# Kernel tuning notes

Hardware: AMD Instinct MI355X
Metric: run time of the kernel (lower is better)

## Reference

```python
import jax, jax.numpy as jnp
import numpy as np

NUM_CLASSES = 80
IGNORE_THRESH = 0.7
LOG_FLOOR = 1e-30  # guards log(0); only hit at masked positions where the BCE term is exactly zero


def _iou_cxcywh(a, b):
    # a: (N,4), b: (M,4), boxes as (cx,cy,w,h) -> IoU (N,M)
    tl = jnp.maximum(a[:, None, :2] - a[:, None, 2:] * 0.5,
                     b[None, :, :2] - b[None, :, 2:] * 0.5)
    br = jnp.minimum(a[:, None, :2] + a[:, None, 2:] * 0.5,
                     b[None, :, :2] + b[None, :, 2:] * 0.5)
    area_a = a[:, 2] * a[:, 3]
    area_b = b[:, 2] * b[:, 3]
    en = jnp.all(tl < br, axis=2).astype(a.dtype)
    area_i = jnp.prod(br - tl, axis=2) * en
    return area_i / (area_a[:, None] + area_b[None, :] - area_i)


def _safelog(x):
    return jnp.log(jnp.maximum(x, LOG_FLOOR))


def _bce_sum(p, t, w=None):
    l = -(t * _safelog(p) + (1.0 - t) * _safelog(1.0 - p))
    if w is not None:
        l = l * w
    return jnp.sum(l)


def _make_pred_boxes(outputs, masked_anchors, ref_anchors):
    B, C, H, W = outputs.shape
    A = masked_anchors.shape[0]
    nc = C // A - 5
    o = outputs.reshape(B, A, 5 + nc, H, W).transpose(0, 1, 3, 4, 2)  # (B,A,H,W,5+nc)
    xs = jnp.arange(W, dtype=o.dtype)
    ys = jnp.arange(H, dtype=o.dtype)
    bx = jax.nn.sigmoid(o[..., 0]) + xs[None, None, None, :]
    by = jax.nn.sigmoid(o[..., 1]) + ys[None, None, :, None]
    bw = jnp.exp(o[..., 2]) * masked_anchors[:, 0][None, :, None, None]
    bh = jnp.exp(o[..., 3]) * masked_anchors[:, 1][None, :, None, None]
    pred = jnp.stack([bx, by, bw, bh], axis=-1)             # (B,A,H,W,4)
    pred = pred.transpose(0, 2, 3, 1, 4).reshape(B, H * W, A, 4)
    gx, gy = jnp.meshgrid(xs, ys)                            # (H,W)
    grid = jnp.stack([gx, gy], axis=-1).reshape(H * W, 1, 2)
    masked_x1y1 = jnp.concatenate(
        [jnp.broadcast_to(grid, (H * W, A, 2)),
         jnp.broadcast_to(masked_anchors[None], (H * W, A, 2))], axis=-1)
    R = ref_anchors.shape[0]
    ref_grid = jnp.concatenate(
        [jnp.broadcast_to(grid, (H * W, R, 2)),
         jnp.broadcast_to(ref_anchors[None], (H * W, R, 2))], axis=-1)
    return pred, masked_x1y1, ref_grid


def _build_targets_one(pred_boxes, gt, num_obj, masked_x1y1, ref_xcyc, anchor_mask, H, W):
    HW = H * W
    A = masked_x1y1.shape[1]
    M = gt.shape[0]
    dtype = pred_boxes.dtype
    gt_boxes = gt[:, :4] * jnp.array([W, H, W, H], dtype=dtype)
    gt_cls = jnp.clip(gt[:, 4].astype(jnp.int32), 0, NUM_CLASSES - 1)
    valid = jnp.arange(M) < num_obj

    ious = _iou_cxcywh(pred_boxes.reshape(-1, 4), gt_boxes)  # (HW*A, M)
    ious = jnp.where(valid[None, :], ious, -1.0)
    max_iou = jnp.max(ious.reshape(HW, A, M), axis=-1)       # (HW, A)

    n_pos = jnp.sum(max_iou > IGNORE_THRESH)
    iou_mask0 = jnp.ones((HW, A), dtype)
    iou_mask0 = jnp.where((n_pos > 0) & (max_iou >= IGNORE_THRESH),
                          jnp.zeros((), dtype), iou_mask0)

    R = ref_xcyc.shape[1]
    ref_ious = _iou_cxcywh(ref_xcyc.reshape(-1, 4), gt_boxes).reshape(HW, R, M)

    init = dict(
        iou_target=jnp.zeros((HW, A), dtype),
        iou_mask=iou_mask0,
        box_target=jnp.zeros((HW, A, 4), dtype),
        box_mask=jnp.zeros((HW, A), dtype),
        box_scale=jnp.zeros((HW, A, 2), dtype),
        class_target=jnp.zeros((HW, A, NUM_CLASSES), dtype),
        class_mask=jnp.zeros((HW, A), dtype),
    )

    one = jnp.ones((), dtype)

    def body(state, xs):
        gt_box, cls_i, v, ref_iou_obj = xs       # ref_iou_obj: (HW, R)
        cx = jnp.floor(gt_box[0]).astype(jnp.int32)
        cy = jnp.floor(gt_box[1]).astype(jnp.int32)
        cell = jnp.clip(cy * W + cx, 0, HW - 1)
        aidx = jnp.argmax(ref_iou_obj[cell])
        do = v & jnp.any(aidx == anchor_mask)
        a3 = aidx % 3
        resp = masked_x1y1[cell, a3]
        delta = jnp.stack([gt_box[0] - resp[0], gt_box[1] - resp[1],
                           gt_box[2] / resp[2], gt_box[3] / resp[3]])
        scale = jnp.sqrt(2.0 - gt_box[2] * gt_box[3] / W / H)

        def upd(arr, new):
            old = arr[cell, a3]
            return arr.at[cell, a3].set(jnp.where(do, new, old))

        new_state = dict(
            iou_target=upd(state['iou_target'], max_iou[cell, a3]),
            iou_mask=upd(state['iou_mask'], one),
            box_target=upd(state['box_target'], delta),
            box_mask=upd(state['box_mask'], one),
            box_scale=upd(state['box_scale'], jnp.stack([scale, scale])),
            class_target=state['class_target'].at[cell, a3, cls_i].set(
                jnp.where(do, one, state['class_target'][cell, a3, cls_i])),
            class_mask=upd(state['class_mask'], one),
        )
        return new_state, None

    xs = (gt_boxes, gt_cls, valid, jnp.moveaxis(ref_ious, -1, 0))
    state, _ = jax.lax.scan(body, init, xs)
    state['iou_mask'] = jnp.where(num_obj == 0, jnp.zeros((), dtype), state['iou_mask'])
    return state


def _forward_loss(outputs, targets, masked_anchors, ref_anchors, anchor_mask):
    B, C, H, W = outputs.shape
    A = masked_anchors.shape[0]
    nc = NUM_CLASSES
    det = jax.lax.stop_gradient(outputs)  # torch: build_targets(outputs.detach().clone(), ...)
    pred_boxes, masked_x1y1, ref_grid = _make_pred_boxes(det, masked_anchors, ref_anchors)
    # faithful to torch's (H*W,3,12) view: +0.5 hits x,y of ref anchors 0,3,6 only
    ref_xcyc = ref_grid.at[:, 0::3, :2].add(0.5)
    gt_num = jnp.sum(jnp.sum(targets, axis=2) > 0, axis=1)
    am = jnp.asarray(anchor_mask, dtype=jnp.int32)
    build = lambda pb, gt, n: _build_targets_one(pb, gt, n, masked_x1y1, ref_xcyc, am, H, W)
    bt = jax.vmap(build)(pred_boxes, targets, gt_num)

    o = outputs.reshape(B, A, 5 + nc, H, W).transpose(0, 3, 4, 1, 2).reshape(B, -1, 5 + nc)
    txy = jax.nn.sigmoid(o[..., :2])
    twh = jnp.exp(o[..., 2:4])
    conf = jax.nn.sigmoid(o[..., 4])
    probs = jax.nn.sigmoid(o[..., 5:])

    box_mask = bt['box_mask'].reshape(-1, 1)
    box_target = bt['box_target'].reshape(-1, 4) * box_mask
    box_scale = bt['box_scale'].reshape(-1, 2) * box_mask
    pred_deltas = jnp.concatenate([txy, twh], -1).reshape(-1, 4) * box_mask

    box_xy_loss = _bce_sum(pred_deltas[:, :2], box_target[:, :2], w=box_scale * box_scale)
    box_wh_loss = jnp.sum((pred_deltas[:, 2:] * box_scale - box_target[:, 2:] * box_scale) ** 2) / 2.0

    iou_mask = bt['iou_mask'].reshape(-1)
    pred_confs = conf.reshape(-1) * iou_mask
    iou_target = bt['iou_target'].reshape(-1) * iou_mask
    iou_loss = _bce_sum(pred_confs, iou_target)

    class_mask = (bt['class_mask'].reshape(-1, 1) > 0).astype(outputs.dtype)
    pred_probs = probs.reshape(-1, nc) * class_mask
    class_target = bt['class_target'].reshape(-1, nc) * class_mask
    class_loss = _bce_sum(pred_probs, class_target)

    return box_xy_loss + box_wh_loss + iou_loss + class_loss


def setup_inputs() -> dict:
    key = jax.random.key(0)
    k1, k2, k3, k4, k5 = jax.random.split(key, 5)
    B, A, H, W, M = 16, 3, 85, 85, 50
    C = A * (5 + NUM_CLASSES)
    outputs = jax.random.normal(k1, (B, C, H, W), jnp.float32)
    cxcy = jax.random.uniform(k2, (B, M, 2), jnp.float32, 0.05, 0.95)
    wh = jax.random.uniform(k3, (B, M, 2), jnp.float32, 0.05, 0.4)
    cls = jax.random.randint(k4, (B, M, 1), 0, NUM_CLASSES).astype(jnp.float32)
    targets = jnp.concatenate([cxcy, wh, cls], axis=-1)
    nobj = jax.random.randint(k5, (B,), 0, M + 1)
    valid = (jnp.arange(M)[None, :] < nobj[:, None]).astype(jnp.float32)
    targets = targets * valid[..., None]
    anchors = jnp.array([[10, 13], [16, 30], [33, 23], [30, 61], [62, 45],
                         [59, 119], [116, 90], [156, 198], [373, 326]], jnp.float32)
    stride = 8.0
    ref_anchors = anchors / stride
    masked_anchors = ref_anchors[:3]
    anchor_mask = jnp.array([0, 1, 2], jnp.int32)
    return {'outputs': outputs, 'targets': targets, 'masked_anchors': masked_anchors,
            'ref_anchors': ref_anchors, 'anchor_mask': anchor_mask}


def reference(outputs, targets, masked_anchors, ref_anchors, anchor_mask):
    return _forward_loss(outputs, targets, masked_anchors, ref_anchors, anchor_mask)
```

## Files before the change

### kernel.cpp

```cpp
#include <hip/hip_runtime.h>
#include <math.h>

#define NUM_CLASSES 80
#define BB 16
#define AA 3
#define HH 85
#define WW 85
#define HW (HH*WW)
#define MM 50
#define CH (AA*(5+NUM_CLASSES))
#define BX ((HW + 255)/256)
#define NBA (BB*AA)
#define NBLK (BX*NBA)

__device__ __forceinline__ float sigmoidf_(float x){ return 1.0f/(1.0f+expf(-x)); }
__device__ __forceinline__ float softplus_(float x){
    return fmaxf(x, 0.0f) + log1pf(expf(-fabsf(x)));
}
__device__ __forceinline__ double atomicExchD(double* p, double v){
    unsigned long long old = atomicExch((unsigned long long*)p, __double_as_longlong(v));
    return __longlong_as_double(old);
}

__global__ void __launch_bounds__(256) k_all(
        const float* __restrict__ outputs,
        const float* __restrict__ targets,
        const float* __restrict__ masked_anchors,
        const float* __restrict__ ref_anchors,
        const int* __restrict__ anchor_mask,
        char* __restrict__ wsb,
        float* __restrict__ out)
{
    double* acc_l  = (double*)(wsb);
    double* acc_lc = (double*)(wsb + 2048);
    int*    posfl  = (int*)(wsb + 4096);
    unsigned int* colcnt = (unsigned int*)(wsb + 6144);
    unsigned int* cnt    = (unsigned int*)(wsb + 12288);

    __shared__ float s_gx1[MM], s_gy1[MM], s_gx2[MM], s_gy2[MM], s_garea[MM];
    __shared__ float s_delta[MM][4];
    __shared__ float s_scale[MM];
    __shared__ int   s_no;
    __shared__ int   s_win[256];
    __shared__ unsigned int s_cm[256][3];
    __shared__ double s_rl[4], s_rlc[4];
    __shared__ int   s_anyw[4];
    __shared__ int   s_prev;
    __shared__ double s_fa[16], s_fc[16];
    __shared__ int   s_fp[16];

    const int tid  = threadIdx.x;
    const int ba   = blockIdx.y;
    const int b    = ba / AA, a = ba % AA;
    const int base = blockIdx.x << 8;
    const int bid  = ba * BX + blockIdx.x;

    if (tid == 0){
        unsigned int v = __hip_atomic_load(&colcnt[ba*32], __ATOMIC_RELAXED,
                                           __HIP_MEMORY_SCOPE_AGENT);
        if (v >= (unsigned int)BX) atomicCAS(&colcnt[ba*32], v, 0u);
    }

    s_win[tid] = -1;
    s_cm[tid][0] = 0u; s_cm[tid][1] = 0u; s_cm[tid][2] = 0u;

    float g0=0.f,g1=0.f,g2=0.f,g3=0.f,g4=0.f;
    bool gflag = false;
    if (tid < MM){
        const float* g = targets + ((size_t)b*MM + tid)*5;
        g0=g[0]; g1=g[1]; g2=g[2]; g3=g[3]; g4=g[4];
        gflag = (g0+g1+g2+g3+g4) > 0.0f;
    }
    unsigned long long bal = __ballot(gflag);
    if (tid == 0) s_no = __popcll(bal);
    __syncthreads();
    const int no = s_no;

    if (tid < MM){
        float gx = g0*(float)WW, gy = g1*(float)HH, gw = g2*(float)WW, gh = g3*(float)HH;
        int cls = min(max((int)g4, 0), NUM_CLASSES-1);
        bool valid = (tid < no);
        int cx = (int)floorf(gx), cy = (int)floorf(gy);
        int cell = min(max(cy*WW + cx, 0), HW-1);
        float xg = (float)(cell % WW), yg = (float)(cell / WW);
        float gx1 = gx - gw*0.5f, gy1 = gy - gh*0.5f;
        float gx2 = gx + gw*0.5f, gy2 = gy + gh*0.5f;
        float garea = gw*gh;
        float bai = -1.0f, bun = 1.0f; int aidx = 0;
        for (int r = 0; r < 9; ++r){
            float off = (r % 3 == 0) ? 0.5f : 0.0f;
            float acx = xg + off, acy = yg + off;
            float aw = ref_anchors[2*r], ah = ref_anchors[2*r+1];
            float tlx = fmaxf(acx - aw*0.5f, gx1), tly = fmaxf(acy - ah*0.5f, gy1);
            float brx = fminf(acx + aw*0.5f, gx2), bry = fminf(acy + ah*0.5f, gy2);
            float ai = (tlx < brx && tly < bry) ? (brx - tlx)*(bry - tly) : 0.0f;
            float un = aw*ah + garea - ai;
            if (ai*bun > bai*un){ bai = ai; bun = un; aidx = r; }
        }
        bool dof = valid && (aidx == anchor_mask[0] || aidx == anchor_mask[1] || aidx == anchor_mask[2]);
        int a3 = aidx % 3;
        float mw = masked_anchors[2*a3], mh = masked_anchors[2*a3+1];
        s_gx1[tid] = gx1; s_gy1[tid] = gy1; s_gx2[tid] = gx2; s_gy2[tid] = gy2;
        s_garea[tid] = garea;
        s_delta[tid][0] = gx - xg; s_delta[tid][1] = gy - yg;
        s_delta[tid][2] = gw/mw;   s_delta[tid][3] = gh/mh;
        s_scale[tid] = sqrtf(2.0f - gw*gh/(float)WW/(float)HH);
        if (dof && a3 == a){
            int ci = cell - base;
            if (ci >= 0 && ci < 256){
                atomicMax(&s_win[ci], tid);
                atomicOr(&s_cm[ci][cls >> 5], 1u << (cls & 31));
            }
        }
    }
    __syncthreads();

    double l = 0.0, lc = 0.0;
    bool pos = false;
    const int hw = base + tid;
    if (hw < HW && no > 0){
        int xg = hw % WW, yg = hw / WW;
        size_t obase = ((size_t)(b*CH + a*(5+NUM_CLASSES)))*HW + hw;
        float o0 = outputs[obase];
        float o1 = outputs[obase + HW];
        float o2 = outputs[obase + 2*HW];
        float o3 = outputs[obase + 3*HW];
        float o4 = outputs[obase + 4*HW];
        float px = sigmoidf_(o0) + (float)xg;
        float py = sigmoidf_(o1) + (float)yg;
        float e2 = expf(o2), e3 = expf(o3);
        float pw = e2*masked_anchors[2*a], ph = e3*masked_anchors[2*a+1];
        float px1 = px - pw*0.5f, py1 = py - ph*0.5f;
        float px2 = px + pw*0.5f, py2 = py + ph*0.5f;
        float parea = pw*ph;
        float bax = 0.0f, bun = 1.0f;
        for (int m = 0; m < no; ++m){
            float tlx = fmaxf(px1, s_gx1[m]), tly = fmaxf(py1, s_gy1[m]);
            float brx = fminf(px2, s_gx2[m]), bry = fminf(py2, s_gy2[m]);
            float ai = (tlx < brx && tly < bry) ? (brx - tlx)*(bry - tly) : 0.0f;
            float un = parea + s_garea[m] - ai;
            if (ai*bun > bax*un){ bax = ai; bun = un; }
        }
        pos = (bax > 0.7f*bun);
        int win = s_win[tid];
        float sp4 = softplus_(o4);
        if (win >= 0){
            float mi = bax/bun;
            l += (double)(sp4 - mi*o4);
            float dx = s_delta[win][0], dy = s_delta[win][1];
            float dw = s_delta[win][2], dh = s_delta[win][3];
            float s = s_scale[win];
            float w2 = s*s;
            l += (double)((softplus_(o0) - dx*o0)*w2);
            l += (double)((softplus_(o1) - dy*o1)*w2);
            float d2 = e2*s - dw*s, d3 = e3*s - dh*s;
            l += 0.5*((double)(d2*d2) + (double)(d3*d3));
            unsigned int c0 = s_cm[tid][0], c1 = s_cm[tid][1], c2 = s_cm[tid][2];
            #pragma unroll 8
            for (int c = 0; c < NUM_CLASSES; ++c){
                float oc = outputs[obase + (size_t)(5+c)*HW];
                unsigned int w = (c < 32) ? c0 : ((c < 64) ? c1 : c2);
                float tt = ((w >> (c & 31)) & 1u) ? 1.0f : 0.0f;
                l += (double)(softplus_(oc) - tt*oc);
            }
        } else {
            if (bax >= 0.7f*bun) lc += (double)sp4;
            else                 l  += (double)sp4;
        }
    }

    for (int off = 32; off > 0; off >>= 1){
        l  += __shfl_down(l,  off);
        lc += __shfl_down(lc, off);
    }
    unsigned long long pbal = __ballot(pos);
    int wid = tid >> 6;
    if ((tid & 63) == 0){
        s_rl[wid] = l; s_rlc[wid] = lc; s_anyw[wid] = (pbal != 0ull) ? 1 : 0;
    }
    __syncthreads();
    if (tid == 0){
        double bl  = s_rl[0] + s_rl[1] + s_rl[2] + s_rl[3];
        double blc = s_rlc[0] + s_rlc[1] + s_rlc[2] + s_rlc[3];
        int anyp = s_anyw[0] | s_anyw[1] | s_anyw[2] | s_anyw[3];
        atomicAdd(&acc_l[(bid & 15)*16], bl);
        if (blc != 0.0) atomicAdd(&acc_lc[b*16], blc);
        if (anyp) atomicOr(&posfl[b*32], 1);
        __builtin_amdgcn_s_waitcnt(0);
        int prev = -1;
        unsigned int cp = atomicAdd(&colcnt[ba*32], 1u);
        if (cp == (unsigned int)(BX - 1)){
            unsigned int v = __hip_atomic_load(cnt, __ATOMIC_RELAXED,
                                              __HIP_MEMORY_SCOPE_AGENT);
            if (v >= (unsigned int)NBA) atomicCAS(cnt, v, 0u);
            prev = (int)atomicAdd(cnt, 1u);
        }
        s_prev = prev;
    }
    __syncthreads();

    if (s_prev == NBA - 1){
        if (tid < 16)      s_fa[tid]      = atomicExchD(&acc_l[tid*16], 0.0);
        else if (tid < 32) s_fc[tid - 16] = atomicExchD(&acc_lc[(tid-16)*16], 0.0);
        else if (tid < 48) s_fp[tid - 32] = atomicExch(&posfl[(tid-32)*32], 0);
        else if (tid < 96) atomicExch(&colcnt[(tid-48)*32], 0u);
        __syncthreads();
        if (tid == 0){
            double t = 0.0;
            for (int i = 0; i < 16; ++i) t += s_fa[i];
            for (int bb = 0; bb < BB; ++bb) if (!s_fp[bb]) t += s_fc[bb];
            out[0] = (float)t;
            atomicExch(cnt, 0u);
        }
    }
}

extern "C" void kernel_launch(void* const* d_in, const int* in_sizes, int n_in,
                              void* d_out, int out_size, void* d_ws, size_t ws_size,
                              hipStream_t stream) {
    const float* outputs        = (const float*)d_in[0];
    const float* targets        = (const float*)d_in[1];
    const float* masked_anchors = (const float*)d_in[2];
    const float* ref_anchors    = (const float*)d_in[3];
    const int*   anchor_mask    = (const int*)d_in[4];

    dim3 grid(BX, NBA);
    k_all<<<grid, 256, 0, stream>>>(outputs, targets, masked_anchors, ref_anchors,
                                    anchor_mask, (char*)d_ws, (float*)d_out);
}
```

Baseline: 21.09 us.

## Use division-free IoU threshold test, float4 shared boxes, and 512-thread blocks

Replaces the per-pixel best-IoU tracking loop with a division-free threshold test (1.7*inter - 0.7*(area_p+area_g) > 0). The exact max-IoU is recomputed only for the few positive-target pixels. Ground-truth boxes and deltas are packed into float4 shared arrays so each iteration needs fewer LDS reads, and the block size doubles to 512 threads, halving the block count and the atomic traffic per column. The fma-based threshold can differ slightly from the original comparison at boundary cases, and the larger blocks lower the grid's granularity.

```diff
diff --git a/kernel.cpp b/kernel.cpp
--- a/kernel.cpp
+++ b/kernel.cpp
@@ -9,7 +9,8 @@
 #define HW (HH*WW)
 #define MM 50
 #define CH (AA*(5+NUM_CLASSES))
-#define BX ((HW + 255)/256)
+#define TPB 512
+#define BX ((HW + TPB - 1)/TPB)
 #define NBA (BB*AA)
 #define NBLK (BX*NBA)
 
@@ -22,7 +23,7 @@
     return __longlong_as_double(old);
 }
 
-__global__ void __launch_bounds__(256) k_all(
+__global__ void __launch_bounds__(TPB) k_all(
         const float* __restrict__ outputs,
         const float* __restrict__ targets,
         const float* __restrict__ masked_anchors,
@@ -37,22 +38,23 @@
     unsigned int* colcnt = (unsigned int*)(wsb + 6144);
     unsigned int* cnt    = (unsigned int*)(wsb + 12288);
 
-    __shared__ float s_gx1[MM], s_gy1[MM], s_gx2[MM], s_gy2[MM], s_garea[MM];
-    __shared__ float s_delta[MM][4];
-    __shared__ float s_scale[MM];
-    __shared__ int   s_no;
-    __shared__ int   s_win[256];
-    __shared__ unsigned int s_cm[256][3];
-    __shared__ double s_rl[4], s_rlc[4];
-    __shared__ int   s_anyw[4];
-    __shared__ int   s_prev;
+    __shared__ float4 s_gbox[MM];
+    __shared__ float  s_ga[MM];
+    __shared__ float4 s_dd[MM];
+    __shared__ float  s_scale[MM];
+    __shared__ int    s_no;
+    __shared__ int    s_win[TPB];
+    __shared__ unsigned int s_cm[TPB][3];
+    __shared__ double s_rl[8], s_rlc[8];
+    __shared__ int    s_anyw[8];
+    __shared__ int    s_prev;
     __shared__ double s_fa[16], s_fc[16];
-    __shared__ int   s_fp[16];
+    __shared__ int    s_fp[16];
 
     const int tid  = threadIdx.x;
     const int ba   = blockIdx.y;
     const int b    = ba / AA, a = ba % AA;
-    const int base = blockIdx.x << 8;
+    const int base = blockIdx.x * TPB;
     const int bid  = ba * BX + blockIdx.x;
 
     if (tid == 0){
@@ -91,23 +93,22 @@
             float off = (r % 3 == 0) ? 0.5f : 0.0f;
             float acx = xg + off, acy = yg + off;
             float aw = ref_anchors[2*r], ah = ref_anchors[2*r+1];
-            float tlx = fmaxf(acx - aw*0.5f, gx1), tly = fmaxf(acy - ah*0.5f, gy1);
-            float brx = fminf(acx + aw*0.5f, gx2), bry = fminf(acy + ah*0.5f, gy2);
-            float ai = (tlx < brx && tly < bry) ? (brx - tlx)*(bry - tly) : 0.0f;
+            float w = fminf(acx + aw*0.5f, gx2) - fmaxf(acx - aw*0.5f, gx1);
+            float h = fminf(acy + ah*0.5f, gy2) - fmaxf(acy - ah*0.5f, gy1);
+            float ai = fmaxf(w, 0.0f)*fmaxf(h, 0.0f);
             float un = aw*ah + garea - ai;
             if (ai*bun > bai*un){ bai = ai; bun = un; aidx = r; }
         }
         bool dof = valid && (aidx == anchor_mask[0] || aidx == anchor_mask[1] || aidx == anchor_mask[2]);
         int a3 = aidx % 3;
         float mw = masked_anchors[2*a3], mh = masked_anchors[2*a3+1];
-        s_gx1[tid] = gx1; s_gy1[tid] = gy1; s_gx2[tid] = gx2; s_gy2[tid] = gy2;
-        s_garea[tid] = garea;
-        s_delta[tid][0] = gx - xg; s_delta[tid][1] = gy - yg;
-        s_delta[tid][2] = gw/mw;   s_delta[tid][3] = gh/mh;
+        s_gbox[tid] = make_float4(gx1, gy1, gx2, gy2);
+        s_ga[tid] = garea;
+        s_dd[tid] = make_float4(gx - xg, gy - yg, gw/mw, gh/mh);
         s_scale[tid] = sqrtf(2.0f - gw*gh/(float)WW/(float)HH);
         if (dof && a3 == a){
             int ci = cell - base;
-            if (ci >= 0 && ci < 256){
+            if (ci >= 0 && ci < TPB){
                 atomicMax(&s_win[ci], tid);
                 atomicOr(&s_cm[ci][cls >> 5], 1u << (cls & 31));
             }
@@ -132,28 +133,39 @@
         float pw = e2*masked_anchors[2*a], ph = e3*masked_anchors[2*a+1];
         float px1 = px - pw*0.5f, py1 = py - ph*0.5f;
         float px2 = px + pw*0.5f, py2 = py + ph*0.5f;
-        float parea = pw*ph;
-        float bax = 0.0f, bun = 1.0f;
+        float pc = 0.7f*pw*ph;
+        float md = -1.0f;
         for (int m = 0; m < no; ++m){
-            float tlx = fmaxf(px1, s_gx1[m]), tly = fmaxf(py1, s_gy1[m]);
-            float brx = fminf(px2, s_gx2[m]), bry = fminf(py2, s_gy2[m]);
-            float ai = (tlx < brx && tly < bry) ? (brx - tlx)*(bry - tly) : 0.0f;
-            float un = parea + s_garea[m] - ai;
-            if (ai*bun > bax*un){ bax = ai; bun = un; }
-        }
-        pos = (bax > 0.7f*bun);
+            float4 gb = s_gbox[m];
+            float ga = s_ga[m];
+            float w = fminf(px2, gb.z) - fmaxf(px1, gb.x);
+            float h = fminf(py2, gb.w) - fmaxf(py1, gb.y);
+            float ai = fmaxf(w, 0.0f)*fmaxf(h, 0.0f);
+            float thr = fmaf(0.7f, ga, pc);
+            md = fmaxf(md, fmaf(1.7f, ai, -thr));
+        }
+        pos = (md > 0.0f);
         int win = s_win[tid];
         float sp4 = softplus_(o4);
         if (win >= 0){
+            float bax = 0.0f, bun = 1.0f;
+            float parea = pw*ph;
+            for (int m = 0; m < no; ++m){
+                float4 gb = s_gbox[m];
+                float w = fminf(px2, gb.z) - fmaxf(px1, gb.x);
+                float h = fminf(py2, gb.w) - fmaxf(py1, gb.y);
+                float ai = fmaxf(w, 0.0f)*fmaxf(h, 0.0f);
+                float un = parea + s_ga[m] - ai;
+                if (ai*bun > bax*un){ bax = ai; bun = un; }
+            }
             float mi = bax/bun;
             l += (double)(sp4 - mi*o4);
-            float dx = s_delta[win][0], dy = s_delta[win][1];
-            float dw = s_delta[win][2], dh = s_delta[win][3];
+            float4 dd = s_dd[win];
             float s = s_scale[win];
             float w2 = s*s;
-            l += (double)((softplus_(o0) - dx*o0)*w2);
-            l += (double)((softplus_(o1) - dy*o1)*w2);
-            float d2 = e2*s - dw*s, d3 = e3*s - dh*s;
+            l += (double)((softplus_(o0) - dd.x*o0)*w2);
+            l += (double)((softplus_(o1) - dd.y*o1)*w2);
+            float d2 = e2*s - dd.z*s, d3 = e3*s - dd.w*s;
             l += 0.5*((double)(d2*d2) + (double)(d3*d3));
             unsigned int c0 = s_cm[tid][0], c1 = s_cm[tid][1], c2 = s_cm[tid][2];
             #pragma unroll 8
@@ -164,8 +176,8 @@
                 l += (double)(softplus_(oc) - tt*oc);
             }
         } else {
-            if (bax >= 0.7f*bun) lc += (double)sp4;
-            else                 l  += (double)sp4;
+            if (md >= 0.0f) lc += (double)sp4;
+            else            l  += (double)sp4;
         }
     }
 
@@ -180,9 +192,8 @@
     }
     __syncthreads();
     if (tid == 0){
-        double bl  = s_rl[0] + s_rl[1] + s_rl[2] + s_rl[3];
-        double blc = s_rlc[0] + s_rlc[1] + s_rlc[2] + s_rlc[3];
-        int anyp = s_anyw[0] | s_anyw[1] | s_anyw[2] | s_anyw[3];
+        double bl = 0.0, blc = 0.0; int anyp = 0;
+        for (int i = 0; i < 8; ++i){ bl += s_rl[i]; blc += s_rlc[i]; anyp |= s_anyw[i]; }
         atomicAdd(&acc_l[(bid & 15)*16], bl);
         if (blc != 0.0) atomicAdd(&acc_lc[b*16], blc);
         if (anyp) atomicOr(&posfl[b*32], 1);
@@ -225,6 +236,6 @@
     const int*   anchor_mask    = (const int*)d_in[4];
 
     dim3 grid(BX, NBA);
-    k_all<<<grid, 256, 0, stream>>>(outputs, targets, masked_anchors, ref_anchors,
+    k_all<<<grid, TPB, 0, stream>>>(outputs, targets, masked_anchors, ref_anchors,
                                     anchor_mask, (char*)d_ws, (float*)d_out);
 }
```

Result: slower. 27.22 us (+29.1%).
